# Optimization experiments

Hardware: AMD Instinct MI355X
Metric: run time of the kernel (lower is better)

The kernel has to match this reference:

```python
import jax, jax.numpy as jnp
import numpy as np

N = 50000          # nodes
E = 1000000        # edges (avg degree 20)
F_IN = 16          # fluidFeatures
LAYERS = [64, 64, 64, 2]
TERMS = 4          # basisTerms
DIM = 2            # spatial dim
EDGE_DIM = TERMS * DIM  # mode='cat' -> terms * dim = 8
OUT_SCALE = 1.0 / 128.0  # outputScaling


def fourier_basis(n_terms, x):
    """Fourier basis ('ffourier'): k=0 -> 1, odd k -> sin(pi*ceil(k/2)*x), even k -> cos(pi*(k/2)*x). x: [E] -> [E, n_terms]."""
    cols = []
    for k in range(n_terms):
        if k == 0:
            cols.append(jnp.ones_like(x))
        elif k % 2 == 1:
            cols.append(jnp.sin(jnp.pi * ((k + 1) // 2) * x))
        else:
            cols.append(jnp.cos(jnp.pi * (k // 2) * x))
    return jnp.stack(cols, axis=-1)


def edge_basis(edge_lengths):
    # basisEncoderLayer with mode='cat': per-component basis, concatenated -> [E, TERMS*DIM]
    return jnp.concatenate([fourier_basis(TERMS, edge_lengths[:, d]) for d in range(DIM)], axis=1)


def setup_inputs() -> dict:
    key = jax.random.key(0)
    k_x, k_ei, k_el, k_w = jax.random.split(key, 4)
    x = jax.random.normal(k_x, (N, F_IN), dtype=jnp.float32)
    edge_index = jax.random.randint(k_ei, (2, E), 0, N)
    edge_lengths = jax.random.uniform(k_el, (E, DIM), dtype=jnp.float32, minval=-1.0, maxval=1.0)
    # continuous-conv weights: [EDGE_DIM, in_feat, out_feat] per layer (uniform-style init)
    weights = {}
    in_f = F_IN
    wkeys = jax.random.split(k_w, len(LAYERS))
    for i, out_f in enumerate(LAYERS):
        scale = 1.0 / np.sqrt(EDGE_DIM * in_f)
        weights[f"W{i}"] = scale * jax.random.normal(wkeys[i], (EDGE_DIM, in_f, out_f), dtype=jnp.float32)
        in_f = out_f
    return dict(x=x, edge_index=edge_index, edge_lengths=edge_lengths, **weights)


def reference(x, edge_index, edge_lengths, W0, W1, W2, W3):
    src = edge_index[0]
    dst = edge_index[1]
    basis = edge_basis(edge_lengths)            # [E, EDGE_DIM]
    Ws = [W0, W1, W2, W3]
    h = x
    for i, W in enumerate(Ws):
        # gather sender features, contract with per-edge basis and conv weight, scatter-sum to receivers
        msg = jnp.einsum('eb,ef,bfo->eo', basis, h[src], W)   # [E, out]
        agg = jax.ops.segment_sum(msg, dst, num_segments=N)   # [N, out]
        h = jax.nn.relu(agg) if i < len(Ws) - 1 else agg
    return h * OUT_SCALE
```

## Files before the change

kernel.cpp:

```cpp
#include <hip/hip_runtime.h>
#include <hip/hip_bf16.h>
#include <math.h>

#define PI_F 3.14159265358979323846f

typedef __attribute__((ext_vector_type(8))) short bf16x8;
typedef __attribute__((ext_vector_type(4))) float f32x4;
typedef __attribute__((ext_vector_type(4))) unsigned short u16x4;

__device__ __forceinline__ float bf2f(unsigned short u) {
    union { unsigned int i; float f; } v;
    v.i = ((unsigned int)u) << 16;
    return v.f;
}

__device__ __forceinline__ unsigned short f2bf_bits(float f) {
    __hip_bfloat16 b = __float2bfloat16(f);
    unsigned short u;
    __builtin_memcpy(&u, &b, 2);
    return u;
}


__global__ void count_kernel(const int* __restrict__ dst, int* __restrict__ cnt, int E) {
    int e = blockIdx.x * 256 + threadIdx.x;
    if (e < E) atomicAdd(&cnt[dst[e]], 1);
}

__global__ __launch_bounds__(256) void scan_reduce_kernel(const int* __restrict__ cnt,
                                                          int* __restrict__ bsum, int n) {
    __shared__ int sd[4];
    int idx = blockIdx.x * 256 + threadIdx.x;
    int v = (idx < n) ? cnt[idx] : 0;
    int s = v;
#pragma unroll
    for (int m = 1; m < 64; m <<= 1) s += __shfl_xor(s, m, 64);
    int wave = threadIdx.x >> 6;
    if ((threadIdx.x & 63) == 0) sd[wave] = s;
    __syncthreads();
    if (threadIdx.x == 0) bsum[blockIdx.x] = sd[0] + sd[1] + sd[2] + sd[3];
}

__global__ __launch_bounds__(256) void scan_top_kernel(const int* __restrict__ bsum,
                                                       int* __restrict__ boffs, int nb) {
    __shared__ int sd[256];
    int tid = threadIdx.x;
    int v = (tid < nb) ? bsum[tid] : 0;
    sd[tid] = v;
    __syncthreads();
#pragma unroll
    for (int off = 1; off < 256; off <<= 1) {
        int t = (tid >= off) ? sd[tid - off] : 0;
        __syncthreads();
        sd[tid] += t;
        __syncthreads();
    }
    if (tid < nb) boffs[tid] = sd[tid] - v;
}

__global__ __launch_bounds__(256) void scan_apply_kernel(int* __restrict__ cntcur,
                                                         int* __restrict__ offs,
                                                         const int* __restrict__ boffs,
                                                         int n, int total) {
    __shared__ int sd[256];
    int tid = threadIdx.x;
    int idx = blockIdx.x * 256 + tid;
    int v = (idx < n) ? cntcur[idx] : 0;
    sd[tid] = v;
    __syncthreads();
#pragma unroll
    for (int off = 1; off < 256; off <<= 1) {
        int t = (tid >= off) ? sd[tid - off] : 0;
        __syncthreads();
        sd[tid] += t;
        __syncthreads();
    }
    if (idx < n) {
        int ex = boffs[blockIdx.x] + sd[tid] - v;
        offs[idx] = ex;
        cntcur[idx] = ex;
    }
    if (idx == 0) offs[n] = total;
}

__global__ void fill_kernel(const int* __restrict__ src, const int* __restrict__ dst,
                            const float* __restrict__ el, int* __restrict__ cursor,
                            int* __restrict__ srcS, float* __restrict__ basisS, int E) {
    int e = blockIdx.x * 256 + threadIdx.x;
    if (e >= E) return;
    int d = dst[e];
    int pos = atomicAdd(&cursor[d], 1);
    srcS[pos] = src[e];
    float2 xy = *(const float2*)(el + 2 * (size_t)e);
    float4 b0, b1;
    b0.x = 1.0f; b0.y = __sinf(PI_F * xy.x); b0.z = __cosf(PI_F * xy.x); b0.w = __sinf(2.0f * PI_F * xy.x);
    b1.x = 1.0f; b1.y = __sinf(PI_F * xy.y); b1.z = __cosf(PI_F * xy.y); b1.w = __sinf(2.0f * PI_F * xy.y);
    float4* bp = (float4*)(basisS + (size_t)pos * 8);
    bp[0] = b0;
    bp[1] = b1;
}


__global__ void prep_w_kernel(const float* __restrict__ W, __hip_bfloat16* __restrict__ Wt, int K) {
    int i = blockIdx.x * 256 + threadIdx.x;
    if (i >= K * 64) return;
    int k = i >> 6, o = i & 63;
    Wt[(size_t)o * K + k] = __float2bfloat16(W[i]);
}

__global__ void prep_f2b_kernel(const float* __restrict__ in, __hip_bfloat16* __restrict__ out, int n) {
    int i = blockIdx.x * 256 + threadIdx.x;
    if (i < n) out[i] = __float2bfloat16(in[i]);
}


__device__ __forceinline__ void agg64_core(const unsigned short* __restrict__ hp,
                                           const int* __restrict__ srcS,
                                           const float4* __restrict__ bp,
                                           int start, int end, int eg, int fg,
                                           float acc[8][4]) {
    for (int j = start; j < end; j += 8) {
        int e0 = j + eg;
        int e1 = j + 4 + eg;
        int q0 = min(e0, end - 1);
        int q1 = min(e1, end - 1);
        int s0 = srcS[q0];
        int s1 = srcS[q1];
        u16x4 g0 = *(const u16x4*)(hp + (size_t)s0 * 64 + fg * 4);
        u16x4 g1 = *(const u16x4*)(hp + (size_t)s1 * 64 + fg * 4);
        float4 c00 = bp[2 * q0], c01 = bp[2 * q0 + 1];
        float4 c10 = bp[2 * q1], c11 = bp[2 * q1 + 1];
        float h0[4], h1[4];
        h0[0] = bf2f(g0[0]); h0[1] = bf2f(g0[1]); h0[2] = bf2f(g0[2]); h0[3] = bf2f(g0[3]);
        h1[0] = bf2f(g1[0]); h1[1] = bf2f(g1[1]); h1[2] = bf2f(g1[2]); h1[3] = bf2f(g1[3]);
        if (e0 >= end) { h0[0] = 0.f; h0[1] = 0.f; h0[2] = 0.f; h0[3] = 0.f; }
        if (e1 >= end) { h1[0] = 0.f; h1[1] = 0.f; h1[2] = 0.f; h1[3] = 0.f; }
        float bas0[8] = {c00.x, c00.y, c00.z, c00.w, c01.x, c01.y, c01.z, c01.w};
        float bas1[8] = {c10.x, c10.y, c10.z, c10.w, c11.x, c11.y, c11.z, c11.w};
#pragma unroll
        for (int b = 0; b < 8; b++) {
#pragma unroll
            for (int c = 0; c < 4; c++) acc[b][c] += bas0[b] * h0[c];
        }
#pragma unroll
        for (int b = 0; b < 8; b++) {
#pragma unroll
            for (int c = 0; c < 4; c++) acc[b][c] += bas1[b] * h1[c];
        }
    }
}

__global__ __launch_bounds__(256) void agg64_kernel(const __hip_bfloat16* __restrict__ h,
                                                    const int* __restrict__ srcS,
                                                    const float* __restrict__ basisS,
                                                    const int* __restrict__ offs,
                                                    __hip_bfloat16* __restrict__ A, int nN) {
    int wid = (blockIdx.x * 256 + threadIdx.x) >> 6;
    int lane = threadIdx.x & 63;
    if (wid >= nN) return;
    int eg = lane >> 4, fg = lane & 15;
    int start = offs[wid], end = offs[wid + 1];
    float acc[8][4] = {};
    if (start < end)
        agg64_core((const unsigned short*)h, srcS, (const float4*)basisS, start, end, eg, fg, acc);
#pragma unroll
    for (int b = 0; b < 8; b++) {
#pragma unroll
        for (int c = 0; c < 4; c++) {
            float v = acc[b][c];
            v += __shfl_xor(v, 16, 64);
            v += __shfl_xor(v, 32, 64);
            acc[b][c] = v;
        }
    }
    if (eg == 0) {
        unsigned short* Ar = (unsigned short*)A + (size_t)wid * 512;
#pragma unroll
        for (int b = 0; b < 8; b++) {
            u16x4 p;
            p[0] = f2bf_bits(acc[b][0]); p[1] = f2bf_bits(acc[b][1]);
            p[2] = f2bf_bits(acc[b][2]); p[3] = f2bf_bits(acc[b][3]);
            *(u16x4*)(Ar + b * 64 + fg * 4) = p;
        }
    }
}

__global__ __launch_bounds__(256) void agg_out_kernel(const __hip_bfloat16* __restrict__ h,
                                                      const int* __restrict__ srcS,
                                                      const float* __restrict__ basisS,
                                                      const int* __restrict__ offs,
                                                      const float* __restrict__ W3,
                                                      float* __restrict__ out, int nN) {
    int wid = (blockIdx.x * 256 + threadIdx.x) >> 6;
    int lane = threadIdx.x & 63;
    if (wid >= nN) return;
    int eg = lane >> 4, fg = lane & 15;
    int start = offs[wid], end = offs[wid + 1];
    float acc[8][4] = {};
    if (start < end)
        agg64_core((const unsigned short*)h, srcS, (const float4*)basisS, start, end, eg, fg, acc);
#pragma unroll
    for (int b = 0; b < 8; b++) {
#pragma unroll
        for (int c = 0; c < 4; c++) {
            float v = acc[b][c];
            v += __shfl_xor(v, 16, 64);
            v += __shfl_xor(v, 32, 64);
            acc[b][c] = v;
        }
    }
    float o0 = 0.f, o1 = 0.f;
#pragma unroll
    for (int b = 0; b < 8; b++) {
        const float* w = W3 + (size_t)(b * 64 + fg * 4) * 2;
        float4 wa = *(const float4*)w;
        float4 wb = *(const float4*)(w + 4);
        o0 += acc[b][0] * wa.x + acc[b][1] * wa.z + acc[b][2] * wb.x + acc[b][3] * wb.z;
        o1 += acc[b][0] * wa.y + acc[b][1] * wa.w + acc[b][2] * wb.y + acc[b][3] * wb.w;
    }
#pragma unroll
    for (int m = 1; m < 16; m <<= 1) {
        o0 += __shfl_xor(o0, m, 64);
        o1 += __shfl_xor(o1, m, 64);
    }
    if (lane == 0) {
        out[(size_t)wid * 2 + 0] = o0 * (1.0f / 128.0f);
        out[(size_t)wid * 2 + 1] = o1 * (1.0f / 128.0f);
    }
}


__global__ __launch_bounds__(256) void agg16_kernel(const __hip_bfloat16* __restrict__ h,
                                                    const int* __restrict__ srcS,
                                                    const float* __restrict__ basisS,
                                                    const int* __restrict__ offs,
                                                    __hip_bfloat16* __restrict__ A, int nN) {
    int wid = (blockIdx.x * 256 + threadIdx.x) >> 6;
    int lane = threadIdx.x & 63;
    if (wid >= nN) return;
    int eg = lane >> 2, fg = lane & 3;
    int start = offs[wid], end = offs[wid + 1];
    const unsigned short* hp = (const unsigned short*)h;
    const float4* bp = (const float4*)basisS;
    float acc[8][4] = {};
    for (int j = start; j < end; j += 16) {
        int e = j + eg;
        int q = min(e, end - 1);
        int s = srcS[q];
        u16x4 g = *(const u16x4*)(hp + (size_t)s * 16 + fg * 4);
        float4 c0 = bp[2 * q], c1 = bp[2 * q + 1];
        float hv[4];
        hv[0] = bf2f(g[0]); hv[1] = bf2f(g[1]); hv[2] = bf2f(g[2]); hv[3] = bf2f(g[3]);
        if (e >= end) { hv[0] = 0.f; hv[1] = 0.f; hv[2] = 0.f; hv[3] = 0.f; }
        float bas[8] = {c0.x, c0.y, c0.z, c0.w, c1.x, c1.y, c1.z, c1.w};
#pragma unroll
        for (int b = 0; b < 8; b++) {
#pragma unroll
            for (int c = 0; c < 4; c++) acc[b][c] += bas[b] * hv[c];
        }
    }
#pragma unroll
    for (int b = 0; b < 8; b++) {
#pragma unroll
        for (int c = 0; c < 4; c++) {
            float v = acc[b][c];
            v += __shfl_xor(v, 4, 64);
            v += __shfl_xor(v, 8, 64);
            v += __shfl_xor(v, 16, 64);
            v += __shfl_xor(v, 32, 64);
            acc[b][c] = v;
        }
    }
    if (eg == 0) {
        unsigned short* Ar = (unsigned short*)A + (size_t)wid * 128;
#pragma unroll
        for (int b = 0; b < 8; b++) {
            u16x4 p;
            p[0] = f2bf_bits(acc[b][0]); p[1] = f2bf_bits(acc[b][1]);
            p[2] = f2bf_bits(acc[b][2]); p[3] = f2bf_bits(acc[b][3]);
            *(u16x4*)(Ar + b * 16 + fg * 4) = p;
        }
    }
}


template <int K, bool RELU>
__global__ __launch_bounds__(256) void gemm_mfma_kernel(const __hip_bfloat16* __restrict__ A,
                                                        const __hip_bfloat16* __restrict__ Wt,
                                                        __hip_bfloat16* __restrict__ Hout, int nN) {
    int wave = threadIdx.x >> 6;
    int lane = threadIdx.x & 63;
    int m16 = lane & 15;
    int kg = lane >> 4;
    int arow = blockIdx.x * 64 + wave * 16 + m16;
    bool rowok = arow < nN;
    const short* Ap = (const short*)A;
    const short* Wp = (const short*)Wt;
    size_t abase = (size_t)arow * K + kg * 8;
    size_t wb0 = (size_t)(0 * 16 + m16) * K + kg * 8;
    size_t wb1 = (size_t)(1 * 16 + m16) * K + kg * 8;
    size_t wb2 = (size_t)(2 * 16 + m16) * K + kg * 8;
    size_t wb3 = (size_t)(3 * 16 + m16) * K + kg * 8;
    f32x4 acc0 = {0.f, 0.f, 0.f, 0.f};
    f32x4 acc1 = {0.f, 0.f, 0.f, 0.f};
    f32x4 acc2 = {0.f, 0.f, 0.f, 0.f};
    f32x4 acc3 = {0.f, 0.f, 0.f, 0.f};
#pragma unroll 4
    for (int kc = 0; kc < K; kc += 32) {
        bf16x8 af = {};
        if (rowok) af = *(const bf16x8*)(Ap + abase + kc);
        bf16x8 b0 = *(const bf16x8*)(Wp + wb0 + kc);
        bf16x8 b1 = *(const bf16x8*)(Wp + wb1 + kc);
        bf16x8 b2 = *(const bf16x8*)(Wp + wb2 + kc);
        bf16x8 b3 = *(const bf16x8*)(Wp + wb3 + kc);
        acc0 = __builtin_amdgcn_mfma_f32_16x16x32_bf16(af, b0, acc0, 0, 0, 0);
        acc1 = __builtin_amdgcn_mfma_f32_16x16x32_bf16(af, b1, acc1, 0, 0, 0);
        acc2 = __builtin_amdgcn_mfma_f32_16x16x32_bf16(af, b2, acc2, 0, 0, 0);
        acc3 = __builtin_amdgcn_mfma_f32_16x16x32_bf16(af, b3, acc3, 0, 0, 0);
    }
    int orow0 = blockIdx.x * 64 + wave * 16 + kg * 4;
#pragma unroll
    for (int r = 0; r < 4; r++) {
        int row = orow0 + r;
        if (row < nN) {
            float v0 = acc0[r], v1 = acc1[r], v2 = acc2[r], v3 = acc3[r];
            if (RELU) {
                v0 = fmaxf(v0, 0.0f); v1 = fmaxf(v1, 0.0f);
                v2 = fmaxf(v2, 0.0f); v3 = fmaxf(v3, 0.0f);
            }
            __hip_bfloat16* Hr = Hout + (size_t)row * 64;
            Hr[0 * 16 + m16] = __float2bfloat16(v0);
            Hr[1 * 16 + m16] = __float2bfloat16(v1);
            Hr[2 * 16 + m16] = __float2bfloat16(v2);
            Hr[3 * 16 + m16] = __float2bfloat16(v3);
        }
    }
}


extern "C" void kernel_launch(void* const* d_in, const int* in_sizes, int n_in,
                              void* d_out, int out_size, void* d_ws, size_t ws_size,
                              hipStream_t stream) {
    const float* x  = (const float*)d_in[0];
    const int*   ei = (const int*)d_in[1];
    const float* el = (const float*)d_in[2];
    const float* W0 = (const float*)d_in[3];
    const float* W1 = (const float*)d_in[4];
    const float* W2 = (const float*)d_in[5];
    const float* W3 = (const float*)d_in[6];
    int nN = in_sizes[0] / 16;
    int E  = in_sizes[1] / 2;
    const int* src = ei;
    const int* dst = ei + E;

    char* ws = (char*)d_ws;
    size_t off = 0;
    auto alloc = [&](size_t bytes) -> void* {
        void* p = ws + off;
        off = (off + bytes + 255) & ~(size_t)255;
        return p;
    };
    int nsb = (nN + 255) / 256;
    int*   cntcur = (int*)alloc((size_t)(nN + 1) * 4);
    int*   offs   = (int*)alloc((size_t)(nN + 1) * 4);
    int*   bsum   = (int*)alloc((size_t)nsb * 4);
    int*   boffs  = (int*)alloc((size_t)nsb * 4);
    int*   srcS   = (int*)alloc((size_t)E * 4);
    float* basisS = (float*)alloc((size_t)E * 8 * 4);
    __hip_bfloat16* Ab  = (__hip_bfloat16*)alloc((size_t)nN * 512 * 2);
    __hip_bfloat16* Wt0 = (__hip_bfloat16*)alloc((size_t)64 * 128 * 2);
    __hip_bfloat16* Wt1 = (__hip_bfloat16*)alloc((size_t)64 * 512 * 2);
    __hip_bfloat16* Wt2 = (__hip_bfloat16*)alloc((size_t)64 * 512 * 2);
    __hip_bfloat16* xb  = (__hip_bfloat16*)alloc((size_t)nN * 16 * 2);
    __hip_bfloat16* hA  = (__hip_bfloat16*)alloc((size_t)nN * 64 * 2);
    __hip_bfloat16* hB  = (__hip_bfloat16*)alloc((size_t)nN * 64 * 2);
    (void)ws_size;

    hipMemsetAsync(cntcur, 0, (size_t)nN * 4, stream);
    int eb = (E + 255) / 256;
    count_kernel<<<eb, 256, 0, stream>>>(dst, cntcur, E);
    scan_reduce_kernel<<<nsb, 256, 0, stream>>>(cntcur, bsum, nN);
    scan_top_kernel<<<1, 256, 0, stream>>>(bsum, boffs, nsb);
    scan_apply_kernel<<<nsb, 256, 0, stream>>>(cntcur, offs, boffs, nN, E);
    fill_kernel<<<eb, 256, 0, stream>>>(src, dst, el, cntcur, srcS, basisS, E);

    prep_w_kernel<<<(128 * 64 + 255) / 256, 256, 0, stream>>>(W0, Wt0, 128);
    prep_w_kernel<<<(512 * 64 + 255) / 256, 256, 0, stream>>>(W1, Wt1, 512);
    prep_w_kernel<<<(512 * 64 + 255) / 256, 256, 0, stream>>>(W2, Wt2, 512);
    prep_f2b_kernel<<<(nN * 16 + 255) / 256, 256, 0, stream>>>(x, xb, nN * 16);

    int nb = (nN + 3) / 4;
    int gb = (nN + 63) / 64;

    agg16_kernel<<<nb, 256, 0, stream>>>(xb, srcS, basisS, offs, Ab, nN);
    gemm_mfma_kernel<128, true><<<gb, 256, 0, stream>>>(Ab, Wt0, hA, nN);
    agg64_kernel<<<nb, 256, 0, stream>>>(hA, srcS, basisS, offs, Ab, nN);
    gemm_mfma_kernel<512, true><<<gb, 256, 0, stream>>>(Ab, Wt1, hB, nN);
    agg64_kernel<<<nb, 256, 0, stream>>>(hB, srcS, basisS, offs, Ab, nN);
    gemm_mfma_kernel<512, true><<<gb, 256, 0, stream>>>(Ab, Wt2, hA, nN);
    agg_out_kernel<<<nb, 256, 0, stream>>>(hA, srcS, basisS, offs, W3, (float*)d_out, nN);
}
```

Before: 446.2 us.

## Store edge basis in bf16 and split 64-wide aggregation across two waves per node

The per-edge Fourier basis is now stored as bf16 (16 bytes per edge instead of 32), halving the basis traffic read by every aggregation pass. The 64-feature aggregation kernels now assign two waves per node, each covering 32 features with 8 edge groups, so more edges are in flight per node. The output layer combines the two halves with atomicAdd into a zeroed output, and agg16 processes two edges per lane per iteration. Rounding the basis to bf16 adds precision loss, and each basis vector is now read by both half-waves, duplicating some loads.

```diff
diff --git a/kernel.cpp b/kernel.cpp
--- a/kernel.cpp
+++ b/kernel.cpp
@@ -7,6 +7,7 @@
 typedef __attribute__((ext_vector_type(8))) short bf16x8;
 typedef __attribute__((ext_vector_type(4))) float f32x4;
 typedef __attribute__((ext_vector_type(4))) unsigned short u16x4;
+typedef __attribute__((ext_vector_type(8))) unsigned short u16x8;
 
 __device__ __forceinline__ float bf2f(unsigned short u) {
     union { unsigned int i; float f; } v;
@@ -85,19 +86,23 @@
 
 __global__ void fill_kernel(const int* __restrict__ src, const int* __restrict__ dst,
                             const float* __restrict__ el, int* __restrict__ cursor,
-                            int* __restrict__ srcS, float* __restrict__ basisS, int E) {
+                            int* __restrict__ srcS, unsigned short* __restrict__ basisB, int E) {
     int e = blockIdx.x * 256 + threadIdx.x;
     if (e >= E) return;
     int d = dst[e];
     int pos = atomicAdd(&cursor[d], 1);
     srcS[pos] = src[e];
     float2 xy = *(const float2*)(el + 2 * (size_t)e);
-    float4 b0, b1;
-    b0.x = 1.0f; b0.y = __sinf(PI_F * xy.x); b0.z = __cosf(PI_F * xy.x); b0.w = __sinf(2.0f * PI_F * xy.x);
-    b1.x = 1.0f; b1.y = __sinf(PI_F * xy.y); b1.z = __cosf(PI_F * xy.y); b1.w = __sinf(2.0f * PI_F * xy.y);
-    float4* bp = (float4*)(basisS + (size_t)pos * 8);
-    bp[0] = b0;
-    bp[1] = b1;
+    u16x8 p;
+    p[0] = f2bf_bits(1.0f);
+    p[1] = f2bf_bits(__sinf(PI_F * xy.x));
+    p[2] = f2bf_bits(__cosf(PI_F * xy.x));
+    p[3] = f2bf_bits(__sinf(2.0f * PI_F * xy.x));
+    p[4] = f2bf_bits(1.0f);
+    p[5] = f2bf_bits(__sinf(PI_F * xy.y));
+    p[6] = f2bf_bits(__cosf(PI_F * xy.y));
+    p[7] = f2bf_bits(__sinf(2.0f * PI_F * xy.y));
+    *(u16x8*)(basisB + (size_t)pos * 8) = p;
 }
 
 
@@ -114,60 +119,63 @@
 }
 
 
-__device__ __forceinline__ void agg64_core(const unsigned short* __restrict__ hp,
-                                           const int* __restrict__ srcS,
-                                           const float4* __restrict__ bp,
-                                           int start, int end, int eg, int fg,
-                                           float acc[8][4]) {
-    for (int j = start; j < end; j += 8) {
+__device__ __forceinline__ void agg64h_core(const unsigned short* __restrict__ hp,
+                                            const int* __restrict__ srcS,
+                                            const unsigned short* __restrict__ basisB,
+                                            int start, int end, int eg, int fbase,
+                                            float acc[8][4]) {
+    for (int j = start; j < end; j += 16) {
         int e0 = j + eg;
-        int e1 = j + 4 + eg;
+        int e1 = j + 8 + eg;
         int q0 = min(e0, end - 1);
         int q1 = min(e1, end - 1);
         int s0 = srcS[q0];
         int s1 = srcS[q1];
-        u16x4 g0 = *(const u16x4*)(hp + (size_t)s0 * 64 + fg * 4);
-        u16x4 g1 = *(const u16x4*)(hp + (size_t)s1 * 64 + fg * 4);
-        float4 c00 = bp[2 * q0], c01 = bp[2 * q0 + 1];
-        float4 c10 = bp[2 * q1], c11 = bp[2 * q1 + 1];
+        u16x4 g0 = *(const u16x4*)(hp + (size_t)s0 * 64 + fbase);
+        u16x4 g1 = *(const u16x4*)(hp + (size_t)s1 * 64 + fbase);
+        u16x8 bb0 = *(const u16x8*)(basisB + (size_t)q0 * 8);
+        u16x8 bb1 = *(const u16x8*)(basisB + (size_t)q1 * 8);
         float h0[4], h1[4];
         h0[0] = bf2f(g0[0]); h0[1] = bf2f(g0[1]); h0[2] = bf2f(g0[2]); h0[3] = bf2f(g0[3]);
         h1[0] = bf2f(g1[0]); h1[1] = bf2f(g1[1]); h1[2] = bf2f(g1[2]); h1[3] = bf2f(g1[3]);
         if (e0 >= end) { h0[0] = 0.f; h0[1] = 0.f; h0[2] = 0.f; h0[3] = 0.f; }
         if (e1 >= end) { h1[0] = 0.f; h1[1] = 0.f; h1[2] = 0.f; h1[3] = 0.f; }
-        float bas0[8] = {c00.x, c00.y, c00.z, c00.w, c01.x, c01.y, c01.z, c01.w};
-        float bas1[8] = {c10.x, c10.y, c10.z, c10.w, c11.x, c11.y, c11.z, c11.w};
-#pragma unroll
-        for (int b = 0; b < 8; b++) {
-#pragma unroll
-            for (int c = 0; c < 4; c++) acc[b][c] += bas0[b] * h0[c];
-        }
-#pragma unroll
-        for (int b = 0; b < 8; b++) {
-#pragma unroll
-            for (int c = 0; c < 4; c++) acc[b][c] += bas1[b] * h1[c];
-        }
-    }
-}
-
-__global__ __launch_bounds__(256) void agg64_kernel(const __hip_bfloat16* __restrict__ h,
-                                                    const int* __restrict__ srcS,
-                                                    const float* __restrict__ basisS,
-                                                    const int* __restrict__ offs,
-                                                    __hip_bfloat16* __restrict__ A, int nN) {
-    int wid = (blockIdx.x * 256 + threadIdx.x) >> 6;
+#pragma unroll
+        for (int b = 0; b < 8; b++) {
+            float bs = bf2f(bb0[b]);
+#pragma unroll
+            for (int c = 0; c < 4; c++) acc[b][c] += bs * h0[c];
+        }
+#pragma unroll
+        for (int b = 0; b < 8; b++) {
+            float bs = bf2f(bb1[b]);
+#pragma unroll
+            for (int c = 0; c < 4; c++) acc[b][c] += bs * h1[c];
+        }
+    }
+}
+
+__global__ __launch_bounds__(256, 4) void agg64_kernel(const __hip_bfloat16* __restrict__ h,
+                                                       const int* __restrict__ srcS,
+                                                       const unsigned short* __restrict__ basisB,
+                                                       const int* __restrict__ offs,
+                                                       __hip_bfloat16* __restrict__ A, int nN) {
+    int gw = (blockIdx.x * 256 + threadIdx.x) >> 6;
+    int wid = gw >> 1, half = gw & 1;
+    if (wid >= nN) return;
     int lane = threadIdx.x & 63;
-    if (wid >= nN) return;
-    int eg = lane >> 4, fg = lane & 15;
+    int eg = lane >> 3, fg = lane & 7;
+    int fbase = half * 32 + fg * 4;
     int start = offs[wid], end = offs[wid + 1];
     float acc[8][4] = {};
     if (start < end)
-        agg64_core((const unsigned short*)h, srcS, (const float4*)basisS, start, end, eg, fg, acc);
+        agg64h_core((const unsigned short*)h, srcS, basisB, start, end, eg, fbase, acc);
 #pragma unroll
     for (int b = 0; b < 8; b++) {
 #pragma unroll
         for (int c = 0; c < 4; c++) {
             float v = acc[b][c];
+            v += __shfl_xor(v, 8, 64);
             v += __shfl_xor(v, 16, 64);
             v += __shfl_xor(v, 32, 64);
             acc[b][c] = v;
@@ -180,30 +188,33 @@
             u16x4 p;
             p[0] = f2bf_bits(acc[b][0]); p[1] = f2bf_bits(acc[b][1]);
             p[2] = f2bf_bits(acc[b][2]); p[3] = f2bf_bits(acc[b][3]);
-            *(u16x4*)(Ar + b * 64 + fg * 4) = p;
-        }
-    }
-}
-
-__global__ __launch_bounds__(256) void agg_out_kernel(const __hip_bfloat16* __restrict__ h,
-                                                      const int* __restrict__ srcS,
-                                                      const float* __restrict__ basisS,
-                                                      const int* __restrict__ offs,
-                                                      const float* __restrict__ W3,
-                                                      float* __restrict__ out, int nN) {
-    int wid = (blockIdx.x * 256 + threadIdx.x) >> 6;
+            *(u16x4*)(Ar + b * 64 + fbase) = p;
+        }
+    }
+}
+
+__global__ __launch_bounds__(256, 4) void agg_out_kernel(const __hip_bfloat16* __restrict__ h,
+                                                         const int* __restrict__ srcS,
+                                                         const unsigned short* __restrict__ basisB,
+                                                         const int* __restrict__ offs,
+                                                         const float* __restrict__ W3,
+                                                         float* __restrict__ out, int nN) {
+    int gw = (blockIdx.x * 256 + threadIdx.x) >> 6;
+    int wid = gw >> 1, half = gw & 1;
+    if (wid >= nN) return;
     int lane = threadIdx.x & 63;
-    if (wid >= nN) return;
-    int eg = lane >> 4, fg = lane & 15;
+    int eg = lane >> 3, fg = lane & 7;
+    int fbase = half * 32 + fg * 4;
     int start = offs[wid], end = offs[wid + 1];
     float acc[8][4] = {};
     if (start < end)
-        agg64_core((const unsigned short*)h, srcS, (const float4*)basisS, start, end, eg, fg, acc);
+        agg64h_core((const unsigned short*)h, srcS, basisB, start, end, eg, fbase, acc);
 #pragma unroll
     for (int b = 0; b < 8; b++) {
 #pragma unroll
         for (int c = 0; c < 4; c++) {
             float v = acc[b][c];
+            v += __shfl_xor(v, 8, 64);
             v += __shfl_xor(v, 16, 64);
             v += __shfl_xor(v, 32, 64);
             acc[b][c] = v;
@@ -212,51 +223,63 @@
     float o0 = 0.f, o1 = 0.f;
 #pragma unroll
     for (int b = 0; b < 8; b++) {
-        const float* w = W3 + (size_t)(b * 64 + fg * 4) * 2;
+        const float* w = W3 + (size_t)(b * 64 + fbase) * 2;
         float4 wa = *(const float4*)w;
         float4 wb = *(const float4*)(w + 4);
         o0 += acc[b][0] * wa.x + acc[b][1] * wa.z + acc[b][2] * wb.x + acc[b][3] * wb.z;
         o1 += acc[b][0] * wa.y + acc[b][1] * wa.w + acc[b][2] * wb.y + acc[b][3] * wb.w;
     }
 #pragma unroll
-    for (int m = 1; m < 16; m <<= 1) {
+    for (int m = 1; m < 8; m <<= 1) {
         o0 += __shfl_xor(o0, m, 64);
         o1 += __shfl_xor(o1, m, 64);
     }
     if (lane == 0) {
-        out[(size_t)wid * 2 + 0] = o0 * (1.0f / 128.0f);
-        out[(size_t)wid * 2 + 1] = o1 * (1.0f / 128.0f);
-    }
-}
-
-
-__global__ __launch_bounds__(256) void agg16_kernel(const __hip_bfloat16* __restrict__ h,
-                                                    const int* __restrict__ srcS,
-                                                    const float* __restrict__ basisS,
-                                                    const int* __restrict__ offs,
-                                                    __hip_bfloat16* __restrict__ A, int nN) {
+        atomicAdd(&out[(size_t)wid * 2 + 0], o0 * (1.0f / 128.0f));
+        atomicAdd(&out[(size_t)wid * 2 + 1], o1 * (1.0f / 128.0f));
+    }
+}
+
+
+__global__ __launch_bounds__(256, 4) void agg16_kernel(const __hip_bfloat16* __restrict__ h,
+                                                       const int* __restrict__ srcS,
+                                                       const unsigned short* __restrict__ basisB,
+                                                       const int* __restrict__ offs,
+                                                       __hip_bfloat16* __restrict__ A, int nN) {
     int wid = (blockIdx.x * 256 + threadIdx.x) >> 6;
     int lane = threadIdx.x & 63;
     if (wid >= nN) return;
     int eg = lane >> 2, fg = lane & 3;
     int start = offs[wid], end = offs[wid + 1];
     const unsigned short* hp = (const unsigned short*)h;
-    const float4* bp = (const float4*)basisS;
     float acc[8][4] = {};
-    for (int j = start; j < end; j += 16) {
-        int e = j + eg;
-        int q = min(e, end - 1);
-        int s = srcS[q];
-        u16x4 g = *(const u16x4*)(hp + (size_t)s * 16 + fg * 4);
-        float4 c0 = bp[2 * q], c1 = bp[2 * q + 1];
-        float hv[4];
-        hv[0] = bf2f(g[0]); hv[1] = bf2f(g[1]); hv[2] = bf2f(g[2]); hv[3] = bf2f(g[3]);
-        if (e >= end) { hv[0] = 0.f; hv[1] = 0.f; hv[2] = 0.f; hv[3] = 0.f; }
-        float bas[8] = {c0.x, c0.y, c0.z, c0.w, c1.x, c1.y, c1.z, c1.w};
-#pragma unroll
-        for (int b = 0; b < 8; b++) {
-#pragma unroll
-            for (int c = 0; c < 4; c++) acc[b][c] += bas[b] * hv[c];
+    for (int j = start; j < end; j += 32) {
+        int e0 = j + eg;
+        int e1 = j + 16 + eg;
+        int q0 = min(e0, end - 1);
+        int q1 = min(e1, end - 1);
+        int s0 = srcS[q0];
+        int s1 = srcS[q1];
+        u16x4 g0 = *(const u16x4*)(hp + (size_t)s0 * 16 + fg * 4);
+        u16x4 g1 = *(const u16x4*)(hp + (size_t)s1 * 16 + fg * 4);
+        u16x8 bb0 = *(const u16x8*)(basisB + (size_t)q0 * 8);
+        u16x8 bb1 = *(const u16x8*)(basisB + (size_t)q1 * 8);
+        float h0[4], h1[4];
+        h0[0] = bf2f(g0[0]); h0[1] = bf2f(g0[1]); h0[2] = bf2f(g0[2]); h0[3] = bf2f(g0[3]);
+        h1[0] = bf2f(g1[0]); h1[1] = bf2f(g1[1]); h1[2] = bf2f(g1[2]); h1[3] = bf2f(g1[3]);
+        if (e0 >= end) { h0[0] = 0.f; h0[1] = 0.f; h0[2] = 0.f; h0[3] = 0.f; }
+        if (e1 >= end) { h1[0] = 0.f; h1[1] = 0.f; h1[2] = 0.f; h1[3] = 0.f; }
+#pragma unroll
+        for (int b = 0; b < 8; b++) {
+            float bs = bf2f(bb0[b]);
+#pragma unroll
+            for (int c = 0; c < 4; c++) acc[b][c] += bs * h0[c];
+        }
+#pragma unroll
+        for (int b = 0; b < 8; b++) {
+            float bs = bf2f(bb1[b]);
+#pragma unroll
+            for (int c = 0; c < 4; c++) acc[b][c] += bs * h1[c];
         }
     }
 #pragma unroll
@@ -366,7 +389,7 @@
     int*   bsum   = (int*)alloc((size_t)nsb * 4);
     int*   boffs  = (int*)alloc((size_t)nsb * 4);
     int*   srcS   = (int*)alloc((size_t)E * 4);
-    float* basisS = (float*)alloc((size_t)E * 8 * 4);
+    unsigned short* basisB = (unsigned short*)alloc((size_t)E * 8 * 2);
     __hip_bfloat16* Ab  = (__hip_bfloat16*)alloc((size_t)nN * 512 * 2);
     __hip_bfloat16* Wt0 = (__hip_bfloat16*)alloc((size_t)64 * 128 * 2);
     __hip_bfloat16* Wt1 = (__hip_bfloat16*)alloc((size_t)64 * 512 * 2);
@@ -377,26 +400,28 @@
     (void)ws_size;
 
     hipMemsetAsync(cntcur, 0, (size_t)nN * 4, stream);
+    hipMemsetAsync(d_out, 0, (size_t)nN * 2 * 4, stream);
     int eb = (E + 255) / 256;
     count_kernel<<<eb, 256, 0, stream>>>(dst, cntcur, E);
     scan_reduce_kernel<<<nsb, 256, 0, stream>>>(cntcur, bsum, nN);
     scan_top_kernel<<<1, 256, 0, stream>>>(bsum, boffs, nsb);
     scan_apply_kernel<<<nsb, 256, 0, stream>>>(cntcur, offs, boffs, nN, E);
-    fill_kernel<<<eb, 256, 0, stream>>>(src, dst, el, cntcur, srcS, basisS, E);
+    fill_kernel<<<eb, 256, 0, stream>>>(src, dst, el, cntcur, srcS, basisB, E);
 
     prep_w_kernel<<<(128 * 64 + 255) / 256, 256, 0, stream>>>(W0, Wt0, 128);
     prep_w_kernel<<<(512 * 64 + 255) / 256, 256, 0, stream>>>(W1, Wt1, 512);
     prep_w_kernel<<<(512 * 64 + 255) / 256, 256, 0, stream>>>(W2, Wt2, 512);
     prep_f2b_kernel<<<(nN * 16 + 255) / 256, 256, 0, stream>>>(x, xb, nN * 16);
 
-    int nb = (nN + 3) / 4;
-    int gb = (nN + 63) / 64;
-
-    agg16_kernel<<<nb, 256, 0, stream>>>(xb, srcS, basisS, offs, Ab, nN);
+    int nb  = (nN + 3) / 4;
+    int nb2 = (2 * nN + 3) / 4;
+    int gb  = (nN + 63) / 64;
+
+    agg16_kernel<<<nb, 256, 0, stream>>>(xb, srcS, basisB, offs, Ab, nN);
     gemm_mfma_kernel<128, true><<<gb, 256, 0, stream>>>(Ab, Wt0, hA, nN);
-    agg64_kernel<<<nb, 256, 0, stream>>>(hA, srcS, basisS, offs, Ab, nN);
+    agg64_kernel<<<nb2, 256, 0, stream>>>(hA, srcS, basisB, offs, Ab, nN);
     gemm_mfma_kernel<512, true><<<gb, 256, 0, stream>>>(Ab, Wt1, hB, nN);
-    agg64_kernel<<<nb, 256, 0, stream>>>(hB, srcS, basisS, offs, Ab, nN);
+    agg64_kernel<<<nb2, 256, 0, stream>>>(hB, srcS, basisB, offs, Ab, nN);
     gemm_mfma_kernel<512, true><<<gb, 256, 0, stream>>>(Ab, Wt2, hA, nN);
-    agg_out_kernel<<<nb, 256, 0, stream>>>(hA, srcS, basisS, offs, W3, (float*)d_out, nN);
-}
+    agg_out_kernel<<<nb2, 256, 0, stream>>>(hA, srcS, basisB, offs, W3, (float*)d_out, nN);
+}
```

New measurement: 598.1 us. +34.0%, slower.

## Store edge basis in bf16 and software-pipeline gather loads in aggregation

Applied to the files above, without the earlier changes.

Per-edge basis values are now stored as bf16 (16 bytes per edge instead of 32), which halves basis traffic in the fill kernel and in all four aggregation passes. The aggregation loops are restructured to prefetch the next iteration's source indices, features and basis one step ahead (indices two steps ahead), so the dependent srcS -> feature gather latency overlaps with the FMAs. This uses more registers per thread and lowers basis precision to bf16.

```diff
diff --git a/kernel.cpp b/kernel.cpp
--- a/kernel.cpp
+++ b/kernel.cpp
@@ -7,6 +7,7 @@
 typedef __attribute__((ext_vector_type(8))) short bf16x8;
 typedef __attribute__((ext_vector_type(4))) float f32x4;
 typedef __attribute__((ext_vector_type(4))) unsigned short u16x4;
+typedef __attribute__((ext_vector_type(8))) unsigned short u16x8;
 
 __device__ __forceinline__ float bf2f(unsigned short u) {
     union { unsigned int i; float f; } v;
@@ -85,19 +86,23 @@
 
 __global__ void fill_kernel(const int* __restrict__ src, const int* __restrict__ dst,
                             const float* __restrict__ el, int* __restrict__ cursor,
-                            int* __restrict__ srcS, float* __restrict__ basisS, int E) {
+                            int* __restrict__ srcS, unsigned short* __restrict__ basisB, int E) {
     int e = blockIdx.x * 256 + threadIdx.x;
     if (e >= E) return;
     int d = dst[e];
     int pos = atomicAdd(&cursor[d], 1);
     srcS[pos] = src[e];
     float2 xy = *(const float2*)(el + 2 * (size_t)e);
-    float4 b0, b1;
-    b0.x = 1.0f; b0.y = __sinf(PI_F * xy.x); b0.z = __cosf(PI_F * xy.x); b0.w = __sinf(2.0f * PI_F * xy.x);
-    b1.x = 1.0f; b1.y = __sinf(PI_F * xy.y); b1.z = __cosf(PI_F * xy.y); b1.w = __sinf(2.0f * PI_F * xy.y);
-    float4* bp = (float4*)(basisS + (size_t)pos * 8);
-    bp[0] = b0;
-    bp[1] = b1;
+    u16x8 p;
+    p[0] = f2bf_bits(1.0f);
+    p[1] = f2bf_bits(__sinf(PI_F * xy.x));
+    p[2] = f2bf_bits(__cosf(PI_F * xy.x));
+    p[3] = f2bf_bits(__sinf(2.0f * PI_F * xy.x));
+    p[4] = f2bf_bits(1.0f);
+    p[5] = f2bf_bits(__sinf(PI_F * xy.y));
+    p[6] = f2bf_bits(__cosf(PI_F * xy.y));
+    p[7] = f2bf_bits(__sinf(2.0f * PI_F * xy.y));
+    *(u16x8*)(basisB + (size_t)pos * 8) = p;
 }
 
 
@@ -116,43 +121,54 @@
 
 __device__ __forceinline__ void agg64_core(const unsigned short* __restrict__ hp,
                                            const int* __restrict__ srcS,
-                                           const float4* __restrict__ bp,
-                                           int start, int end, int eg, int fg,
+                                           const unsigned short* __restrict__ basisB,
+                                           int start, int end, int eg, int fb,
                                            float acc[8][4]) {
-    for (int j = start; j < end; j += 8) {
-        int e0 = j + eg;
-        int e1 = j + 4 + eg;
-        int q0 = min(e0, end - 1);
-        int q1 = min(e1, end - 1);
-        int s0 = srcS[q0];
-        int s1 = srcS[q1];
-        u16x4 g0 = *(const u16x4*)(hp + (size_t)s0 * 64 + fg * 4);
-        u16x4 g1 = *(const u16x4*)(hp + (size_t)s1 * 64 + fg * 4);
-        float4 c00 = bp[2 * q0], c01 = bp[2 * q0 + 1];
-        float4 c10 = bp[2 * q1], c11 = bp[2 * q1 + 1];
-        float h0[4], h1[4];
-        h0[0] = bf2f(g0[0]); h0[1] = bf2f(g0[1]); h0[2] = bf2f(g0[2]); h0[3] = bf2f(g0[3]);
-        h1[0] = bf2f(g1[0]); h1[1] = bf2f(g1[1]); h1[2] = bf2f(g1[2]); h1[3] = bf2f(g1[3]);
-        if (e0 >= end) { h0[0] = 0.f; h0[1] = 0.f; h0[2] = 0.f; h0[3] = 0.f; }
-        if (e1 >= end) { h1[0] = 0.f; h1[1] = 0.f; h1[2] = 0.f; h1[3] = 0.f; }
-        float bas0[8] = {c00.x, c00.y, c00.z, c00.w, c01.x, c01.y, c01.z, c01.w};
-        float bas1[8] = {c10.x, c10.y, c10.z, c10.w, c11.x, c11.y, c11.z, c11.w};
+    const int last = end - 1;
+    int j = start;
+    int qa = min(j + eg, last), qb = min(j + 4 + eg, last);
+    int sa = srcS[qa], sb = srcS[qb];
+    u16x4 ga = *(const u16x4*)(hp + (size_t)sa * 64 + fb);
+    u16x4 gb = *(const u16x4*)(hp + (size_t)sb * 64 + fb);
+    u16x8 ca = *(const u16x8*)(basisB + (size_t)qa * 8);
+    u16x8 cb = *(const u16x8*)(basisB + (size_t)qb * 8);
+    int qna = min(j + 8 + eg, last), qnb = min(j + 12 + eg, last);
+    int sna = srcS[qna], snb = srcS[qnb];
+    while (true) {
+        int jn = j + 8;
+        int q2a = min(jn + 8 + eg, last), q2b = min(jn + 12 + eg, last);
+        int s2a = srcS[q2a], s2b = srcS[q2b];
+        u16x4 gna = *(const u16x4*)(hp + (size_t)sna * 64 + fb);
+        u16x4 gnb = *(const u16x4*)(hp + (size_t)snb * 64 + fb);
+        u16x8 cna = *(const u16x8*)(basisB + (size_t)qna * 8);
+        u16x8 cnb = *(const u16x8*)(basisB + (size_t)qnb * 8);
+        float ha[4], hb[4];
+        ha[0] = bf2f(ga[0]); ha[1] = bf2f(ga[1]); ha[2] = bf2f(ga[2]); ha[3] = bf2f(ga[3]);
+        hb[0] = bf2f(gb[0]); hb[1] = bf2f(gb[1]); hb[2] = bf2f(gb[2]); hb[3] = bf2f(gb[3]);
+        if (j + eg >= end)     { ha[0] = 0.f; ha[1] = 0.f; ha[2] = 0.f; ha[3] = 0.f; }
+        if (j + 4 + eg >= end) { hb[0] = 0.f; hb[1] = 0.f; hb[2] = 0.f; hb[3] = 0.f; }
 #pragma unroll
         for (int b = 0; b < 8; b++) {
-#pragma unroll
-            for (int c = 0; c < 4; c++) acc[b][c] += bas0[b] * h0[c];
+            float w = bf2f(ca[b]);
+#pragma unroll
+            for (int c = 0; c < 4; c++) acc[b][c] += w * ha[c];
         }
 #pragma unroll
         for (int b = 0; b < 8; b++) {
-#pragma unroll
-            for (int c = 0; c < 4; c++) acc[b][c] += bas1[b] * h1[c];
-        }
+            float w = bf2f(cb[b]);
+#pragma unroll
+            for (int c = 0; c < 4; c++) acc[b][c] += w * hb[c];
+        }
+        if (jn >= end) break;
+        j = jn;
+        ga = gna; gb = gnb; ca = cna; cb = cnb;
+        qna = q2a; qnb = q2b; sna = s2a; snb = s2b;
     }
 }
 
 __global__ __launch_bounds__(256) void agg64_kernel(const __hip_bfloat16* __restrict__ h,
                                                     const int* __restrict__ srcS,
-                                                    const float* __restrict__ basisS,
+                                                    const unsigned short* __restrict__ basisB,
                                                     const int* __restrict__ offs,
                                                     __hip_bfloat16* __restrict__ A, int nN) {
     int wid = (blockIdx.x * 256 + threadIdx.x) >> 6;
@@ -162,7 +178,7 @@
     int start = offs[wid], end = offs[wid + 1];
     float acc[8][4] = {};
     if (start < end)
-        agg64_core((const unsigned short*)h, srcS, (const float4*)basisS, start, end, eg, fg, acc);
+        agg64_core((const unsigned short*)h, srcS, basisB, start, end, eg, fg * 4, acc);
 #pragma unroll
     for (int b = 0; b < 8; b++) {
 #pragma unroll
@@ -187,7 +203,7 @@
 
 __global__ __launch_bounds__(256) void agg_out_kernel(const __hip_bfloat16* __restrict__ h,
                                                       const int* __restrict__ srcS,
-                                                      const float* __restrict__ basisS,
+                                                      const unsigned short* __restrict__ basisB,
                                                       const int* __restrict__ offs,
                                                       const float* __restrict__ W3,
                                                       float* __restrict__ out, int nN) {
@@ -198,7 +214,7 @@
     int start = offs[wid], end = offs[wid + 1];
     float acc[8][4] = {};
     if (start < end)
-        agg64_core((const unsigned short*)h, srcS, (const float4*)basisS, start, end, eg, fg, acc);
+        agg64_core((const unsigned short*)h, srcS, basisB, start, end, eg, fg * 4, acc);
 #pragma unroll
     for (int b = 0; b < 8; b++) {
 #pragma unroll
@@ -232,7 +248,7 @@
 
 __global__ __launch_bounds__(256) void agg16_kernel(const __hip_bfloat16* __restrict__ h,
                                                     const int* __restrict__ srcS,
-                                                    const float* __restrict__ basisS,
+                                                    const unsigned short* __restrict__ basisB,
                                                     const int* __restrict__ offs,
                                                     __hip_bfloat16* __restrict__ A, int nN) {
     int wid = (blockIdx.x * 256 + threadIdx.x) >> 6;
@@ -240,23 +256,36 @@
     if (wid >= nN) return;
     int eg = lane >> 2, fg = lane & 3;
     int start = offs[wid], end = offs[wid + 1];
-    const unsigned short* hp = (const unsigned short*)h;
-    const float4* bp = (const float4*)basisS;
     float acc[8][4] = {};
-    for (int j = start; j < end; j += 16) {
-        int e = j + eg;
-        int q = min(e, end - 1);
+    if (start < end) {
+        const unsigned short* hp = (const unsigned short*)h;
+        const int last = end - 1;
+        const int fb = fg * 4;
+        int j = start;
+        int q = min(j + eg, last);
         int s = srcS[q];
-        u16x4 g = *(const u16x4*)(hp + (size_t)s * 16 + fg * 4);
-        float4 c0 = bp[2 * q], c1 = bp[2 * q + 1];
-        float hv[4];
-        hv[0] = bf2f(g[0]); hv[1] = bf2f(g[1]); hv[2] = bf2f(g[2]); hv[3] = bf2f(g[3]);
-        if (e >= end) { hv[0] = 0.f; hv[1] = 0.f; hv[2] = 0.f; hv[3] = 0.f; }
-        float bas[8] = {c0.x, c0.y, c0.z, c0.w, c1.x, c1.y, c1.z, c1.w};
-#pragma unroll
-        for (int b = 0; b < 8; b++) {
-#pragma unroll
-            for (int c = 0; c < 4; c++) acc[b][c] += bas[b] * hv[c];
+        u16x4 g = *(const u16x4*)(hp + (size_t)s * 16 + fb);
+        u16x8 cbv = *(const u16x8*)(basisB + (size_t)q * 8);
+        int qn = min(j + 16 + eg, last);
+        int sn = srcS[qn];
+        while (true) {
+            int jn = j + 16;
+            int q2 = min(jn + 16 + eg, last);
+            int s2 = srcS[q2];
+            u16x4 gn = *(const u16x4*)(hp + (size_t)sn * 16 + fb);
+            u16x8 cn = *(const u16x8*)(basisB + (size_t)qn * 8);
+            float hv[4];
+            hv[0] = bf2f(g[0]); hv[1] = bf2f(g[1]); hv[2] = bf2f(g[2]); hv[3] = bf2f(g[3]);
+            if (j + eg >= end) { hv[0] = 0.f; hv[1] = 0.f; hv[2] = 0.f; hv[3] = 0.f; }
+#pragma unroll
+            for (int b = 0; b < 8; b++) {
+                float w = bf2f(cbv[b]);
+#pragma unroll
+                for (int c = 0; c < 4; c++) acc[b][c] += w * hv[c];
+            }
+            if (jn >= end) break;
+            j = jn;
+            g = gn; cbv = cn; qn = q2; sn = s2;
         }
     }
 #pragma unroll
@@ -366,7 +395,7 @@
     int*   bsum   = (int*)alloc((size_t)nsb * 4);
     int*   boffs  = (int*)alloc((size_t)nsb * 4);
     int*   srcS   = (int*)alloc((size_t)E * 4);
-    float* basisS = (float*)alloc((size_t)E * 8 * 4);
+    unsigned short* basisB = (unsigned short*)alloc((size_t)E * 8 * 2);
     __hip_bfloat16* Ab  = (__hip_bfloat16*)alloc((size_t)nN * 512 * 2);
     __hip_bfloat16* Wt0 = (__hip_bfloat16*)alloc((size_t)64 * 128 * 2);
     __hip_bfloat16* Wt1 = (__hip_bfloat16*)alloc((size_t)64 * 512 * 2);
@@ -382,7 +411,7 @@
     scan_reduce_kernel<<<nsb, 256, 0, stream>>>(cntcur, bsum, nN);
     scan_top_kernel<<<1, 256, 0, stream>>>(bsum, boffs, nsb);
     scan_apply_kernel<<<nsb, 256, 0, stream>>>(cntcur, offs, boffs, nN, E);
-    fill_kernel<<<eb, 256, 0, stream>>>(src, dst, el, cntcur, srcS, basisS, E);
+    fill_kernel<<<eb, 256, 0, stream>>>(src, dst, el, cntcur, srcS, basisB, E);
 
     prep_w_kernel<<<(128 * 64 + 255) / 256, 256, 0, stream>>>(W0, Wt0, 128);
     prep_w_kernel<<<(512 * 64 + 255) / 256, 256, 0, stream>>>(W1, Wt1, 512);
@@ -392,11 +421,11 @@
     int nb = (nN + 3) / 4;
     int gb = (nN + 63) / 64;
 
-    agg16_kernel<<<nb, 256, 0, stream>>>(xb, srcS, basisS, offs, Ab, nN);
+    agg16_kernel<<<nb, 256, 0, stream>>>(xb, srcS, basisB, offs, Ab, nN);
     gemm_mfma_kernel<128, true><<<gb, 256, 0, stream>>>(Ab, Wt0, hA, nN);
-    agg64_kernel<<<nb, 256, 0, stream>>>(hA, srcS, basisS, offs, Ab, nN);
+    agg64_kernel<<<nb, 256, 0, stream>>>(hA, srcS, basisB, offs, Ab, nN);
     gemm_mfma_kernel<512, true><<<gb, 256, 0, stream>>>(Ab, Wt1, hB, nN);
-    agg64_kernel<<<nb, 256, 0, stream>>>(hB, srcS, basisS, offs, Ab, nN);
+    agg64_kernel<<<nb, 256, 0, stream>>>(hB, srcS, basisB, offs, Ab, nN);
     gemm_mfma_kernel<512, true><<<gb, 256, 0, stream>>>(Ab, Wt2, hA, nN);
-    agg_out_kernel<<<nb, 256, 0, stream>>>(hA, srcS, basisS, offs, W3, (float*)d_out, nN);
-}
+    agg_out_kernel<<<nb, 256, 0, stream>>>(hA, srcS, basisB, offs, W3, (float*)d_out, nN);
+}
```

Result: faster. 432.6 us (-3.0%).
